# Optimization experiments

Hardware: AMD Instinct MI355X
Metric: run time of the kernel (lower is better)

## Reference

```python
import jax, jax.numpy as jnp
import numpy as np

B, S, D = 2, 2048, 1024
H, HD = 16, 64
FFN_DIM = 4096
EPS = 1e-10


def layer_norm(x, gamma, beta):
    mean = jnp.mean(x, axis=-1, keepdims=True)
    var = jnp.mean((x - mean) ** 2, axis=-1, keepdims=True)
    return (x - mean) / jnp.sqrt(var + EPS) * gamma + beta


def setup_inputs() -> dict:
    key = jax.random.key(0)
    ks = jax.random.split(key, 12)
    s = lambda fan_in, fan_out: (6.0 / (fan_in + fan_out)) ** 0.5
    u = lambda k, shape, c: jax.random.uniform(k, shape, jnp.float32, -c, c)
    return {
        "x": jax.random.normal(ks[0], (B, S, D), jnp.float32),
        "wq": u(ks[1], (H, D, HD), s(D, HD)),
        "bq": jnp.zeros((H, HD), jnp.float32),
        "wk": u(ks[2], (H, D, HD), s(D, HD)),
        "bk": jnp.zeros((H, HD), jnp.float32),
        "wv": u(ks[3], (H, D, HD), s(D, HD)),
        "bv": jnp.zeros((H, HD), jnp.float32),
        "w_proj": u(ks[4], (D, D), s(D, D)),
        "b_proj": jnp.zeros((D,), jnp.float32),
        "gamma1": jnp.ones((D,), jnp.float32),
        "beta1": jnp.zeros((D,), jnp.float32),
        "w1": u(ks[5], (D, FFN_DIM), (1.0 / D) ** 0.5),
        "b1": jnp.zeros((FFN_DIM,), jnp.float32),
        "w2": u(ks[6], (FFN_DIM, D), (1.0 / FFN_DIM) ** 0.5),
        "b2": jnp.zeros((D,), jnp.float32),
        "gamma2": jnp.ones((D,), jnp.float32),
        "beta2": jnp.zeros((D,), jnp.float32),
    }


def reference(x, wq, bq, wk, bk, wv, bv, w_proj, b_proj, gamma1, beta1,
              w1, b1, w2, b2, gamma2, beta2):
    # multi-head self-attention (all heads batched along axis h)
    q = jnp.einsum("bsd,hde->bhse", x, wq) + bq[None, :, None, :]
    k = jnp.einsum("bsd,hde->bhse", x, wk) + bk[None, :, None, :]
    v = jnp.einsum("bsd,hde->bhse", x, wv) + bv[None, :, None, :]
    # scale by sqrt of per-head dim (emb_dim of projected queries)
    scores = jnp.einsum("bhse,bhte->bhst", q, k) / (HD ** 0.5)
    attn = jax.nn.softmax(scores, axis=-1)
    out_h = jnp.einsum("bhst,bhte->bhse", attn, v)  # [B,H,S,HD]
    concat = out_h.transpose(0, 2, 1, 3).reshape(B, S, D)
    attn_out = concat @ w_proj + b_proj
    # residual + norm1 (dropout=0)
    out1 = layer_norm(attn_out + x, gamma1, beta1)
    # FFN: linear - relu - linear
    ffn_out = jax.nn.relu(out1 @ w1 + b1) @ w2 + b2
    # residual + norm2
    return layer_norm(ffn_out + out1, gamma2, beta2)
```

## Files before the change

### kernel.cpp

```cpp
#include <hip/hip_runtime.h>
#include <stdint.h>

typedef float f32x4 __attribute__((ext_vector_type(4)));
typedef __bf16 bf16x8 __attribute__((ext_vector_type(8)));
typedef __bf16 bf16x8_a __attribute__((ext_vector_type(8), may_alias));
typedef __bf16 bf16x4_a __attribute__((ext_vector_type(4), may_alias));
typedef unsigned int u32x4_a __attribute__((ext_vector_type(4), may_alias));
typedef unsigned short u16x4_a __attribute__((ext_vector_type(4), may_alias));

#define DEV __device__ __forceinline__
#define MFMA_B16(a, b, c) __builtin_amdgcn_mfma_f32_16x16x32_bf16((a), (b), (c), 0, 0, 0)

#if __has_builtin(__builtin_amdgcn_exp2f)
#define EXP2(x) __builtin_amdgcn_exp2f(x)
#else
#define EXP2(x) exp2f(x)
#endif

DEV unsigned short f2b(float f) {
  unsigned int u = __float_as_uint(f);
  u = u + 0x7FFFu + ((u >> 16) & 1u);
  return (unsigned short)(u >> 16);
}

#define GLOAD_LDS16(gsrc, ldst)                                                  \
  __builtin_amdgcn_global_load_lds(                                              \
      (__attribute__((address_space(1))) void*)(uintptr_t)(const void*)(gsrc),   \
      (__attribute__((address_space(3))) void*)(ldst), 16, 0, 0)

__global__ __launch_bounds__(256) void cvt_kernel(const float* __restrict__ in,
                                                  unsigned short* __restrict__ out, int n4) {
  int i = blockIdx.x * 256 + threadIdx.x;
  if (i < n4) {
    float4 v = ((const float4*)in)[i];
    u16x4_a t = {f2b(v.x), f2b(v.y), f2b(v.z), f2b(v.w)};
    ((u16x4_a*)out)[i] = t;
  }
}

__global__ __launch_bounds__(256) void transpose_cvt(const float* __restrict__ in,
                                                     unsigned short* __restrict__ out,
                                                     int rows, int cols, float scale) {
  __shared__ float tile[32][33];
  const int tx = threadIdx.x & 31, ty = threadIdx.x >> 5;
  const int c0 = blockIdx.x * 32, r0 = blockIdx.y * 32;
  const float* ip = in + (size_t)blockIdx.z * rows * cols;
  unsigned short* op = out + (size_t)blockIdx.z * rows * cols;
#pragma unroll
  for (int j = 0; j < 32; j += 8)
    tile[ty + j][tx] = ip[(size_t)(r0 + ty + j) * cols + (c0 + tx)];
  __syncthreads();
#pragma unroll
  for (int j = 0; j < 32; j += 8)
    op[(size_t)(c0 + ty + j) * rows + (r0 + tx)] = f2b(tile[tx][ty + j] * scale);
}

__global__ void build_bias_qkv(const float* __restrict__ bq, const float* __restrict__ bk,
                               const float* __restrict__ bv, float* __restrict__ out) {
  int c = blockIdx.x * 256 + threadIdx.x;
  int which = c >> 10, idx = c & 1023;
  float v = which == 0 ? bq[idx] : (which == 1 ? bk[idx] : bv[idx]);
  out[c] = which == 0 ? v * 0.18033688f : v;
}

template <int EP>
__global__ __launch_bounds__(512, 2) void gemm256_kernel(
    const unsigned short* __restrict__ A, const unsigned short* __restrict__ Bt,
    int M, int N, int K, int nbx, int KS,
    const float* __restrict__ bias, unsigned short* __restrict__ outb,
    unsigned short* __restrict__ q_out, unsigned short* __restrict__ k_out,
    unsigned short* __restrict__ v_out,
    float* __restrict__ pp0, float* __restrict__ pp1, float* __restrict__ pp2) {
  __shared__ __align__(16) unsigned short sA[2][256 * 64];
  __shared__ __align__(16) unsigned short sB[2][256 * 64];

  const int tid = threadIdx.x;
  const int wid = tid >> 6, lane = tid & 63;
  const int g = lane >> 4, r15 = lane & 15;
  const int wm = wid >> 2, wn = wid & 3;

  const int nwg = gridDim.x, cpx = nwg >> 3, orig = blockIdx.x;
  const int wg = (orig & 7) * cpx + (orig >> 3);
  const int bx = wg % nbx;
  const int t1 = wg / nbx;
  const int kz = t1 % KS, by = t1 / KS;
  const int row0 = by * 256, col0 = bx * 256;

  const int tilesK = K >> 6;
  const int qT = tilesK / KS, rT = tilesK % KS;
  const int tile0 = kz * qT + (kz < rT ? kz : rT);
  const int NT = qT + (kz < rT ? 1 : 0);
  const int kbase = tile0 << 6;

  const unsigned short* gA0 = A + (size_t)row0 * K + kbase;
  const unsigned short* gB0 = Bt + (size_t)col0 * K + kbase;
  const int srow8 = lane >> 3;
  const int schunk = ((lane & 7) ^ srow8) * 8;

  f32x4 acc[8][4] = {};
  bf16x8 af[4][2], bfr[4][2];

  auto stA = [&](int buf, int k0, int i) {
    const int r = wid * 32 + i * 8;
    GLOAD_LDS16(gA0 + (size_t)(r + srow8) * K + k0 + schunk, &sA[buf][r * 64]);
  };
  auto stB = [&](int buf, int k0, int i) {
    const int r = wid * 32 + i * 8;
    GLOAD_LDS16(gB0 + (size_t)(r + srow8) * K + k0 + schunk, &sB[buf][r * 64]);
  };
  auto ldA = [&](const unsigned short* p, int m, int ks) -> bf16x8 {
    const int row = wm * 128 + m * 16 + r15;
    return *(const bf16x8_a*)&p[row * 64 + (((ks * 4 + g) ^ (r15 & 7)) * 8)];
  };
  auto ldB = [&](const unsigned short* p, int n, int ks) -> bf16x8 {
    const int row = wn * 64 + n * 16 + r15;
    return *(const bf16x8_a*)&p[row * 64 + (((ks * 4 + g) ^ (r15 & 7)) * 8)];
  };

#pragma unroll
  for (int i = 0; i < 4; ++i) { stA(0, 0, i); stB(0, 0, i); }
  asm volatile("s_waitcnt vmcnt(0)" ::: "memory");
  __builtin_amdgcn_s_barrier();

  for (int kt = 0; kt < NT; ++kt) {
    const int cb = kt & 1, nb = cb ^ 1;
    const bool pf = (kt + 1) < NT;
    const int k1 = (kt + 1) << 6;
    const unsigned short* pA = sA[cb];
    const unsigned short* pB = sB[cb];

#pragma unroll
    for (int m = 0; m < 4; ++m) { af[m][0] = ldA(pA, m, 0); af[m][1] = ldA(pA, m, 1); }
#pragma unroll
    for (int n = 0; n < 4; ++n) { bfr[n][0] = ldB(pB, n, 0); bfr[n][1] = ldB(pB, n, 1); }
    if (pf) { stA(nb, k1, 0); stA(nb, k1, 1); }
    __builtin_amdgcn_s_barrier();
    asm volatile("s_waitcnt lgkmcnt(0)" ::: "memory");
    __builtin_amdgcn_sched_barrier(0);
    __builtin_amdgcn_s_setprio(1);
#pragma unroll
    for (int m = 0; m < 4; ++m)
#pragma unroll
      for (int n = 0; n < 2; ++n) {
        acc[m][n] = MFMA_B16(af[m][0], bfr[n][0], acc[m][n]);
        acc[m][n] = MFMA_B16(af[m][1], bfr[n][1], acc[m][n]);
      }
    __builtin_amdgcn_s_setprio(0);
    __builtin_amdgcn_s_barrier();

    if (pf) { stA(nb, k1, 2); stA(nb, k1, 3); }
    __builtin_amdgcn_s_barrier();
    __builtin_amdgcn_s_setprio(1);
#pragma unroll
    for (int m = 0; m < 4; ++m)
#pragma unroll
      for (int n = 2; n < 4; ++n) {
        acc[m][n] = MFMA_B16(af[m][0], bfr[n][0], acc[m][n]);
        acc[m][n] = MFMA_B16(af[m][1], bfr[n][1], acc[m][n]);
      }
    __builtin_amdgcn_s_setprio(0);
    __builtin_amdgcn_s_barrier();

#pragma unroll
    for (int m = 0; m < 4; ++m) { af[m][0] = ldA(pA, m + 4, 0); af[m][1] = ldA(pA, m + 4, 1); }
    if (pf) { stB(nb, k1, 0); stB(nb, k1, 1); }
    __builtin_amdgcn_s_barrier();
    asm volatile("s_waitcnt lgkmcnt(0)" ::: "memory");
    __builtin_amdgcn_sched_barrier(0);
    __builtin_amdgcn_s_setprio(1);
#pragma unroll
    for (int m = 0; m < 4; ++m)
#pragma unroll
      for (int n = 0; n < 2; ++n) {
        acc[m + 4][n] = MFMA_B16(af[m][0], bfr[n][0], acc[m + 4][n]);
        acc[m + 4][n] = MFMA_B16(af[m][1], bfr[n][1], acc[m + 4][n]);
      }
    __builtin_amdgcn_s_setprio(0);
    __builtin_amdgcn_s_barrier();

    if (pf) { stB(nb, k1, 2); stB(nb, k1, 3); }
    __builtin_amdgcn_s_barrier();
    __builtin_amdgcn_s_setprio(1);
#pragma unroll
    for (int m = 0; m < 4; ++m)
#pragma unroll
      for (int n = 2; n < 4; ++n) {
        acc[m + 4][n] = MFMA_B16(af[m][0], bfr[n][0], acc[m + 4][n]);
        acc[m + 4][n] = MFMA_B16(af[m][1], bfr[n][1], acc[m + 4][n]);
      }
    __builtin_amdgcn_s_setprio(0);
    asm volatile("s_waitcnt vmcnt(0)" ::: "memory");
    __builtin_amdgcn_s_barrier();
  }

  float* pz = kz == 0 ? pp0 : (kz == 1 ? pp1 : pp2);
#pragma unroll
  for (int m = 0; m < 8; ++m) {
    const int rbase = row0 + wm * 128 + m * 16 + g * 4;
#pragma unroll
    for (int n = 0; n < 4; ++n) {
      const int col = col0 + wn * 64 + n * 16 + r15;
      const float bb = (EP == 3) ? 0.f : bias[col];
      if constexpr (EP == 0) {
        const int which = col >> 10, cc = col & 1023;
        const int hh = cc >> 6, e = cc & 63;
        const int b = rbase >> 11, s0v = rbase & 2047;
        if (which == 2) {
          bf16x4_a pk;
#pragma unroll
          for (int r = 0; r < 4; ++r) pk[r] = (__bf16)(acc[m][n][r] + bb);
          *(bf16x4_a*)(v_out + (((size_t)(b * 16 + hh) * 64) + e) * 2048 + s0v) = pk;
        } else {
          unsigned short* dst = which == 0 ? q_out : k_out;
#pragma unroll
          for (int r = 0; r < 4; ++r)
            dst[(((size_t)(b * 16 + hh) * 2048) + s0v + r) * 64 + e] =
                f2b(acc[m][n][r] + bb);
        }
      } else {
#pragma unroll
        for (int r = 0; r < 4; ++r) {
          const int row = rbase + r;
          float v = acc[m][n][r] + bb;
          if constexpr (EP == 3) {
            pz[(size_t)row * N + col] = v;
          } else {
            outb[(size_t)row * N + col] = f2b(v > 0.f ? v : 0.f);
          }
        }
      }
    }
  }
}

template <int EP>
__global__ __launch_bounds__(256) void gemm_bt_kernel(
    const unsigned short* __restrict__ A, const unsigned short* __restrict__ Bt,
    int M, int N, int K,
    const float* __restrict__ bias, const float* __restrict__ addf,
    float* __restrict__ outf) {
  __shared__ __align__(16) unsigned short sA[2][128 * 32];
  __shared__ __align__(16) unsigned short sB[2][128 * 32];
  const int tid = threadIdx.x;
  const int wid = tid >> 6, lane = tid & 63;
  const int g = lane >> 4, r15 = lane & 15;
  const int wr = wid >> 1, wc = wid & 1;
  const int row0 = blockIdx.y * 128, col0 = blockIdx.x * 128;

  f32x4 acc[4][4] = {};

  const int c0 = wid * 128 + lane;
  const unsigned short* gA0 = A + (size_t)row0 * K;
  const unsigned short* gB0 = Bt + (size_t)col0 * K;

  auto stage = [&](int buf, int k0) {
#pragma unroll
    for (int j = 0; j < 2; ++j) {
      int c = c0 + j * 64;
      GLOAD_LDS16(gA0 + (size_t)(c >> 2) * K + k0 + (c & 3) * 8,
                  &sA[buf][(wid * 128 + j * 64) * 8]);
      GLOAD_LDS16(gB0 + (size_t)(c >> 2) * K + k0 + (c & 3) * 8,
                  &sB[buf][(wid * 128 + j * 64) * 8]);
    }
  };

  stage(0, 0);
  const int NT = K >> 5;
  for (int t = 0; t < NT; ++t) {
    const int cb = t & 1;
    __syncthreads();
    if (t + 1 < NT) stage(cb ^ 1, (t + 1) * 32);
    bf16x8 af[4], bfr[4];
#pragma unroll
    for (int m = 0; m < 4; ++m)
      af[m] = *(const bf16x8_a*)&sA[cb][(wr * 64 + m * 16 + r15) * 32 + g * 8];
#pragma unroll
    for (int n = 0; n < 4; ++n)
      bfr[n] = *(const bf16x8_a*)&sB[cb][(wc * 64 + n * 16 + r15) * 32 + g * 8];
#pragma unroll
    for (int m = 0; m < 4; ++m)
#pragma unroll
      for (int n = 0; n < 4; ++n)
        acc[m][n] = MFMA_B16(af[m], bfr[n], acc[m][n]);
  }

#pragma unroll
  for (int m = 0; m < 4; ++m) {
    const int rbase = row0 + wr * 64 + m * 16 + g * 4;
#pragma unroll
    for (int n = 0; n < 4; ++n) {
      const int col = col0 + wc * 64 + n * 16 + r15;
      const float bb = bias[col];
#pragma unroll
      for (int r = 0; r < 4; ++r) {
        const int row = rbase + r;
        size_t idx = (size_t)row * N + col;
        outf[idx] = acc[m][n][r] + bb + addf[idx];
      }
    }
  }
}

__global__ __launch_bounds__(256) void attn_kernel(const unsigned short* __restrict__ Q,
                                                   const unsigned short* __restrict__ K,
                                                   const unsigned short* __restrict__ Vt,
                                                   unsigned short* __restrict__ out) {
  const int flat = blockIdx.y * gridDim.x + blockIdx.x;
  const int xcd = flat & 7, rest = flat >> 3;
  const int bh = xcd * 4 + (rest >> 5);
  const int q0 = (rest & 31) * 64;

  const int tid = threadIdx.x, wid = tid >> 6, lane = tid & 63;
  const int g = lane >> 4, r15 = lane & 15;
  const int h = r15 & 7;
  const int s0 = ((g ^ h) * 8);
  const int s1 = (((g + 4) ^ h) * 8);
  const int pswz = r15 & 14;

  __shared__ __align__(16) unsigned short sK[2][64 * 64];
  __shared__ __align__(16) unsigned short sV[2][64 * 64];
  __shared__ __align__(16) unsigned short sP[4][16 * 64];

  const size_t base = (size_t)bh * (2048 * 64);
  const unsigned short* Kb = K + base;
  const unsigned short* Vb = Vt + base;

  const int qrow = q0 + wid * 16 + r15;
  bf16x8 qf[2];
  qf[0] = *(const bf16x8_a*)(Q + base + (size_t)qrow * 64 + g * 8);
  qf[1] = *(const bf16x8_a*)(Q + base + (size_t)qrow * 64 + 32 + g * 8);

  const int srow = lane >> 3;
  const int schunk = ((lane & 7) ^ srow) * 8;

  union {
    unsigned short u[8];
    bf16x8 v;
  } ou;
#pragma unroll
  for (int i = 0; i < 8; ++i) ou.u[i] = 0x3F80;
  const bf16x8 onesb = ou.v;

  f32x4 o[4] = {};
  float mrow = -1e30f, lrow = 0.f;

  auto stage = [&](int bufi, int kt0s) {
#pragma unroll
    for (int i = 0; i < 2; ++i) {
      const int inst = wid * 2 + i;
      const int row = 8 * inst + srow;
      GLOAD_LDS16(Kb + (size_t)(kt0s + row) * 64 + schunk, &sK[bufi][inst * 512]);
      GLOAD_LDS16(Vb + (size_t)row * 2048 + kt0s + schunk, &sV[bufi][inst * 512]);
    }
  };

  stage(0, 0);

  for (int t = 0; t < 32; ++t) {
    const int cur = t & 1;
    __syncthreads();
    if (t < 31) stage(cur ^ 1, (t + 1) * 64);

    f32x4 sc[4] = {};
#pragma unroll
    for (int kt = 0; kt < 4; ++kt) {
      const int rb = (kt * 16 + r15) * 64;
      bf16x8 kf0 = *(const bf16x8_a*)&sK[cur][rb + s0];
      bf16x8 kf1 = *(const bf16x8_a*)&sK[cur][rb + s1];
      sc[kt] = MFMA_B16(kf0, qf[0], sc[kt]);
      sc[kt] = MFMA_B16(kf1, qf[1], sc[kt]);
    }

    float t0 = fmaxf(fmaxf(sc[0][0], sc[0][1]), fmaxf(sc[0][2], sc[0][3]));
    float t1 = fmaxf(fmaxf(sc[1][0], sc[1][1]), fmaxf(sc[1][2], sc[1][3]));
    float t2 = fmaxf(fmaxf(sc[2][0], sc[2][1]), fmaxf(sc[2][2], sc[2][3]));
    float t3 = fmaxf(fmaxf(sc[3][0], sc[3][1]), fmaxf(sc[3][2], sc[3][3]));
    float pmax = fmaxf(fmaxf(t0, t1), fmaxf(t2, t3));
    pmax = fmaxf(pmax, __shfl_xor(pmax, 16));
    pmax = fmaxf(pmax, __shfl_xor(pmax, 32));

    const bool allkeep = __all(pmax - mrow <= 11.5441f);
    float fac;
    if (allkeep) {
      fac = 1.0f;
    } else {
      float nm = fmaxf(mrow, pmax);
      fac = EXP2(mrow - nm);
      mrow = nm;
#pragma unroll
      for (int dt = 0; dt < 4; ++dt)
#pragma unroll
        for (int r = 0; r < 4; ++r) o[dt][r] *= fac;
    }

#pragma unroll
    for (int kt = 0; kt < 4; ++kt) {
      bf16x4_a pb;
      pb[0] = (__bf16)EXP2(sc[kt][0] - mrow);
      pb[1] = (__bf16)EXP2(sc[kt][1] - mrow);
      pb[2] = (__bf16)EXP2(sc[kt][2] - mrow);
      pb[3] = (__bf16)EXP2(sc[kt][3] - mrow);
      *(bf16x4_a*)&sP[wid][r15 * 64 + (((4 * kt + g) ^ pswz) << 2)] = pb;
    }

    bf16x8 pf0 = *(const bf16x8_a*)&sP[wid][r15 * 64 + (((2 * g) ^ pswz) << 2)];
    bf16x8 pf1 = *(const bf16x8_a*)&sP[wid][r15 * 64 + (((8 + 2 * g) ^ pswz) << 2)];

    f32x4 lacc = {};
    lacc = MFMA_B16(onesb, pf0, lacc);
    lacc = MFMA_B16(onesb, pf1, lacc);
    lrow = lrow * fac + lacc[0];

#pragma unroll
    for (int dt = 0; dt < 4; ++dt) {
      const int rb = (dt * 16 + r15) * 64;
      bf16x8 vf0 = *(const bf16x8_a*)&sV[cur][rb + s0];
      bf16x8 vf1 = *(const bf16x8_a*)&sV[cur][rb + s1];
      o[dt] = MFMA_B16(vf0, pf0, o[dt]);
      o[dt] = MFMA_B16(vf1, pf1, o[dt]);
    }
  }

  const int b = bh >> 4, hh = bh & 15;
  const int s = q0 + wid * 16 + r15;
  const float inv = 1.f / lrow;
  unsigned short* orow = out + ((size_t)(b * 2048 + s)) * 1024 + hh * 64;
#pragma unroll
  for (int dt = 0; dt < 4; ++dt) {
    bf16x4_a tq;
    tq[0] = (__bf16)(o[dt][0] * inv);
    tq[1] = (__bf16)(o[dt][1] * inv);
    tq[2] = (__bf16)(o[dt][2] * inv);
    tq[3] = (__bf16)(o[dt][3] * inv);
    *(bf16x4_a*)(orow + dt * 16 + g * 4) = tq;
  }
}

__global__ __launch_bounds__(256) void ln_kernel(const float* __restrict__ in,
                                                 const float* __restrict__ gamma,
                                                 const float* __restrict__ beta,
                                                 float* __restrict__ outf,
                                                 unsigned short* __restrict__ outb) {
  const int row = blockIdx.x, tid = threadIdx.x;
  float4 v = ((const float4*)(in + (size_t)row * 1024))[tid];
  float s = v.x + v.y + v.z + v.w;
  float ss = v.x * v.x + v.y * v.y + v.z * v.z + v.w * v.w;
#pragma unroll
  for (int off = 32; off > 0; off >>= 1) {
    s += __shfl_down(s, off);
    ss += __shfl_down(ss, off);
  }
  __shared__ float red[8];
  const int wid = tid >> 6;
  if ((tid & 63) == 0) { red[wid] = s; red[4 + wid] = ss; }
  __syncthreads();
  float S = red[0] + red[1] + red[2] + red[3];
  float SS = red[4] + red[5] + red[6] + red[7];
  const float mean = S * (1.f / 1024.f);
  const float var = SS * (1.f / 1024.f) - mean * mean;
  const float inv = 1.f / sqrtf(var + 1e-10f);
  float4 gg = ((const float4*)gamma)[tid];
  float4 bb = ((const float4*)beta)[tid];
  float4 o;
  o.x = (v.x - mean) * inv * gg.x + bb.x;
  o.y = (v.y - mean) * inv * gg.y + bb.y;
  o.z = (v.z - mean) * inv * gg.z + bb.z;
  o.w = (v.w - mean) * inv * gg.w + bb.w;
  if (outf) ((float4*)(outf + (size_t)row * 1024))[tid] = o;
  if (outb) {
    u16x4_a t = {f2b(o.x), f2b(o.y), f2b(o.z), f2b(o.w)};
    *(u16x4_a*)(outb + (size_t)row * 1024 + tid * 4) = t;
  }
}

__global__ __launch_bounds__(256) void ln3_kernel(
    const float* __restrict__ p0, const float* __restrict__ p1, const float* __restrict__ p2,
    const float* __restrict__ bias, const float* __restrict__ resid,
    const float* __restrict__ gamma, const float* __restrict__ beta,
    float* __restrict__ outf) {
  const int row = blockIdx.x, tid = threadIdx.x;
  const size_t off = (size_t)row * 1024;
  float4 a = ((const float4*)(p0 + off))[tid];
  float4 b = ((const float4*)(p1 + off))[tid];
  float4 c = ((const float4*)(p2 + off))[tid];
  float4 bb4 = ((const float4*)bias)[tid];
  float4 rr = ((const float4*)(resid + off))[tid];
  float4 v;
  v.x = a.x + b.x + c.x + bb4.x + rr.x;
  v.y = a.y + b.y + c.y + bb4.y + rr.y;
  v.z = a.z + b.z + c.z + bb4.z + rr.z;
  v.w = a.w + b.w + c.w + bb4.w + rr.w;

  float s = v.x + v.y + v.z + v.w;
  float ss = v.x * v.x + v.y * v.y + v.z * v.z + v.w * v.w;
#pragma unroll
  for (int off2 = 32; off2 > 0; off2 >>= 1) {
    s += __shfl_down(s, off2);
    ss += __shfl_down(ss, off2);
  }
  __shared__ float red[8];
  const int wid = tid >> 6;
  if ((tid & 63) == 0) { red[wid] = s; red[4 + wid] = ss; }
  __syncthreads();
  float S = red[0] + red[1] + red[2] + red[3];
  float SS = red[4] + red[5] + red[6] + red[7];
  const float mean = S * (1.f / 1024.f);
  const float var = SS * (1.f / 1024.f) - mean * mean;
  const float inv = 1.f / sqrtf(var + 1e-10f);
  float4 gg = ((const float4*)gamma)[tid];
  float4 be = ((const float4*)beta)[tid];
  float4 o;
  o.x = (v.x - mean) * inv * gg.x + be.x;
  o.y = (v.y - mean) * inv * gg.y + be.y;
  o.z = (v.z - mean) * inv * gg.z + be.z;
  o.w = (v.w - mean) * inv * gg.w + be.w;
  ((float4*)(outf + off))[tid] = o;
}

extern "C" void kernel_launch(void* const* d_in, const int* in_sizes, int n_in,
                              void* d_out, int out_size, void* d_ws, size_t ws_size,
                              hipStream_t stream) {
  const float* x      = (const float*)d_in[0];
  const float* wq     = (const float*)d_in[1];
  const float* bq     = (const float*)d_in[2];
  const float* wk     = (const float*)d_in[3];
  const float* bk     = (const float*)d_in[4];
  const float* wv     = (const float*)d_in[5];
  const float* bv     = (const float*)d_in[6];
  const float* w_proj = (const float*)d_in[7];
  const float* b_proj = (const float*)d_in[8];
  const float* gamma1 = (const float*)d_in[9];
  const float* beta1  = (const float*)d_in[10];
  const float* w1     = (const float*)d_in[11];
  const float* b1     = (const float*)d_in[12];
  const float* w2     = (const float*)d_in[13];
  const float* b2     = (const float*)d_in[14];
  const float* gamma2 = (const float*)d_in[15];
  const float* beta2  = (const float*)d_in[16];

  char* p = (char*)d_ws;
  auto alloc = [&](size_t bytes) {
    char* r = p;
    p += (bytes + 255) & ~(size_t)255;
    return r;
  };
  unsigned short* xb      = (unsigned short*)alloc(4096ull * 1024 * 2);
  unsigned short* Wqkv_t  = (unsigned short*)alloc(3072ull * 1024 * 2);
  unsigned short* Wproj_t = (unsigned short*)alloc(1024ull * 1024 * 2);
  unsigned short* W1t     = (unsigned short*)alloc(4096ull * 1024 * 2);
  unsigned short* W2t     = (unsigned short*)alloc(1024ull * 4096 * 2);
  float*          biasq   = (float*)alloc(3072 * 4);
  unsigned short* Qb      = (unsigned short*)alloc(4096ull * 1024 * 2);
  unsigned short* Kb      = (unsigned short*)alloc(4096ull * 1024 * 2);
  unsigned short* Vtb     = (unsigned short*)alloc(4096ull * 1024 * 2);
  float*          resid1  = (float*)alloc(4096ull * 1024 * 4);
  float*          out1f   = (float*)alloc(4096ull * 1024 * 4);
  unsigned short* out1b   = (unsigned short*)alloc(4096ull * 1024 * 2);
  unsigned short* ffn_h   = (unsigned short*)alloc(4096ull * 4096 * 2);
  unsigned short* concat  = xb;

  float* pp0 = (float*)xb;
  float* pp1 = (float*)Qb;
  float* pp2 = (float*)Vtb;

  cvt_kernel<<<4096, 256, 0, stream>>>(x, xb, 4096 * 1024 / 4);
  transpose_cvt<<<dim3(2, 32, 16), 256, 0, stream>>>(wq, Wqkv_t, 1024, 64, 0.18033688f);
  transpose_cvt<<<dim3(2, 32, 16), 256, 0, stream>>>(wk, Wqkv_t + 1024 * 1024, 1024, 64, 1.f);
  transpose_cvt<<<dim3(2, 32, 16), 256, 0, stream>>>(wv, Wqkv_t + 2048 * 1024, 1024, 64, 1.f);
  transpose_cvt<<<dim3(32, 32, 1), 256, 0, stream>>>(w_proj, Wproj_t, 1024, 1024, 1.f);
  transpose_cvt<<<dim3(128, 32, 1), 256, 0, stream>>>(w1, W1t, 1024, 4096, 1.f);
  transpose_cvt<<<dim3(32, 128, 1), 256, 0, stream>>>(w2, W2t, 4096, 1024, 1.f);
  build_bias_qkv<<<12, 256, 0, stream>>>(bq, bk, bv, biasq);

  gemm256_kernel<0><<<192, 512, 0, stream>>>(xb, Wqkv_t, 4096, 3072, 1024, 12, 1, biasq,
                                             nullptr, Qb, Kb, Vtb, nullptr, nullptr, nullptr);
  attn_kernel<<<dim3(32, 32), 256, 0, stream>>>(Qb, Kb, Vtb, concat);
  gemm_bt_kernel<1><<<dim3(8, 32), 256, 0, stream>>>(concat, Wproj_t, 4096, 1024, 1024, b_proj,
                                                     x, resid1);
  ln_kernel<<<4096, 256, 0, stream>>>(resid1, gamma1, beta1, out1f, out1b);
  gemm256_kernel<2><<<256, 512, 0, stream>>>(out1b, W1t, 4096, 4096, 1024, 16, 1, b1,
                                             ffn_h, nullptr, nullptr, nullptr,
                                             nullptr, nullptr, nullptr);
  gemm256_kernel<3><<<192, 512, 0, stream>>>(ffn_h, W2t, 4096, 1024, 4096, 4, 3, nullptr,
                                             nullptr, nullptr, nullptr, nullptr,
                                             pp0, pp1, pp2);
  ln3_kernel<<<4096, 256, 0, stream>>>(pp0, pp1, pp2, b2, out1f, gamma2, beta2,
                                       (float*)d_out);
}
```

Before: 269.1 us.

## Split-K the output projection and FFN2 GEMMs, fold bias and residual into layernorm

```diff
diff --git a/kernel.cpp b/kernel.cpp
--- a/kernel.cpp
+++ b/kernel.cpp
@@ -70,7 +70,8 @@
     const float* __restrict__ bias, unsigned short* __restrict__ outb,
     unsigned short* __restrict__ q_out, unsigned short* __restrict__ k_out,
     unsigned short* __restrict__ v_out,
-    float* __restrict__ pp0, float* __restrict__ pp1, float* __restrict__ pp2) {
+    float* __restrict__ pp0, float* __restrict__ pp1, float* __restrict__ pp2,
+    float* __restrict__ pp3) {
   __shared__ __align__(16) unsigned short sA[2][256 * 64];
   __shared__ __align__(16) unsigned short sB[2][256 * 64];
 
@@ -193,7 +194,7 @@
     __builtin_amdgcn_s_barrier();
   }
 
-  float* pz = kz == 0 ? pp0 : (kz == 1 ? pp1 : pp2);
+  float* pz = kz == 0 ? pp0 : (kz == 1 ? pp1 : (kz == 2 ? pp2 : pp3));
 #pragma unroll
   for (int m = 0; m < 8; ++m) {
     const int rbase = row0 + wm * 128 + m * 16 + g * 4;
@@ -233,12 +234,10 @@
   }
 }
 
-template <int EP>
 __global__ __launch_bounds__(256) void gemm_bt_kernel(
     const unsigned short* __restrict__ A, const unsigned short* __restrict__ Bt,
-    int M, int N, int K,
-    const float* __restrict__ bias, const float* __restrict__ addf,
-    float* __restrict__ outf) {
+    int M, int N, int Kchunk, int Kstride,
+    float* __restrict__ pp0, float* __restrict__ pp1) {
   __shared__ __align__(16) unsigned short sA[2][128 * 32];
   __shared__ __align__(16) unsigned short sB[2][128 * 32];
   const int tid = threadIdx.x;
@@ -246,26 +245,27 @@
   const int g = lane >> 4, r15 = lane & 15;
   const int wr = wid >> 1, wc = wid & 1;
   const int row0 = blockIdx.y * 128, col0 = blockIdx.x * 128;
+  const int kz = blockIdx.z;
 
   f32x4 acc[4][4] = {};
 
   const int c0 = wid * 128 + lane;
-  const unsigned short* gA0 = A + (size_t)row0 * K;
-  const unsigned short* gB0 = Bt + (size_t)col0 * K;
+  const unsigned short* gA0 = A + (size_t)row0 * Kstride + (size_t)kz * Kchunk;
+  const unsigned short* gB0 = Bt + (size_t)col0 * Kstride + (size_t)kz * Kchunk;
 
   auto stage = [&](int buf, int k0) {
 #pragma unroll
     for (int j = 0; j < 2; ++j) {
       int c = c0 + j * 64;
-      GLOAD_LDS16(gA0 + (size_t)(c >> 2) * K + k0 + (c & 3) * 8,
+      GLOAD_LDS16(gA0 + (size_t)(c >> 2) * Kstride + k0 + (c & 3) * 8,
                   &sA[buf][(wid * 128 + j * 64) * 8]);
-      GLOAD_LDS16(gB0 + (size_t)(c >> 2) * K + k0 + (c & 3) * 8,
+      GLOAD_LDS16(gB0 + (size_t)(c >> 2) * Kstride + k0 + (c & 3) * 8,
                   &sB[buf][(wid * 128 + j * 64) * 8]);
     }
   };
 
   stage(0, 0);
-  const int NT = K >> 5;
+  const int NT = Kchunk >> 5;
   for (int t = 0; t < NT; ++t) {
     const int cb = t & 1;
     __syncthreads();
@@ -284,19 +284,16 @@
         acc[m][n] = MFMA_B16(af[m], bfr[n], acc[m][n]);
   }
 
+  float* pz = kz == 0 ? pp0 : pp1;
 #pragma unroll
   for (int m = 0; m < 4; ++m) {
     const int rbase = row0 + wr * 64 + m * 16 + g * 4;
 #pragma unroll
     for (int n = 0; n < 4; ++n) {
       const int col = col0 + wc * 64 + n * 16 + r15;
-      const float bb = bias[col];
-#pragma unroll
-      for (int r = 0; r < 4; ++r) {
-        const int row = rbase + r;
-        size_t idx = (size_t)row * N + col;
-        outf[idx] = acc[m][n][r] + bb + addf[idx];
-      }
+#pragma unroll
+      for (int r = 0; r < 4; ++r)
+        pz[(size_t)(rbase + r) * N + col] = acc[m][n][r];
     }
   }
 }
@@ -371,11 +368,14 @@
       sc[kt] = MFMA_B16(kf1, qf[1], sc[kt]);
     }
 
-    float t0 = fmaxf(fmaxf(sc[0][0], sc[0][1]), fmaxf(sc[0][2], sc[0][3]));
-    float t1 = fmaxf(fmaxf(sc[1][0], sc[1][1]), fmaxf(sc[1][2], sc[1][3]));
-    float t2 = fmaxf(fmaxf(sc[2][0], sc[2][1]), fmaxf(sc[2][2], sc[2][3]));
-    float t3 = fmaxf(fmaxf(sc[3][0], sc[3][1]), fmaxf(sc[3][2], sc[3][3]));
-    float pmax = fmaxf(fmaxf(t0, t1), fmaxf(t2, t3));
+    float a0 = fmaxf(fmaxf(sc[0][0], sc[0][1]), sc[0][2]);
+    float a1 = fmaxf(fmaxf(sc[0][3], sc[1][0]), sc[1][1]);
+    float a2 = fmaxf(fmaxf(sc[1][2], sc[1][3]), sc[2][0]);
+    float a3 = fmaxf(fmaxf(sc[2][1], sc[2][2]), sc[2][3]);
+    float a4 = fmaxf(fmaxf(sc[3][0], sc[3][1]), sc[3][2]);
+    float b0 = fmaxf(fmaxf(a0, a1), a2);
+    float b1 = fmaxf(fmaxf(a3, a4), sc[3][3]);
+    float pmax = fmaxf(b0, b1);
     pmax = fmaxf(pmax, __shfl_xor(pmax, 16));
     pmax = fmaxf(pmax, __shfl_xor(pmax, 32));
 
@@ -436,19 +436,29 @@
   }
 }
 
-__global__ __launch_bounds__(256) void ln_kernel(const float* __restrict__ in,
-                                                 const float* __restrict__ gamma,
-                                                 const float* __restrict__ beta,
-                                                 float* __restrict__ outf,
-                                                 unsigned short* __restrict__ outb) {
+__global__ __launch_bounds__(256) void ln2p_kernel(
+    const float* __restrict__ p0, const float* __restrict__ p1,
+    const float* __restrict__ bias, const float* __restrict__ resid,
+    const float* __restrict__ gamma, const float* __restrict__ beta,
+    float* __restrict__ outf, unsigned short* __restrict__ outb) {
   const int row = blockIdx.x, tid = threadIdx.x;
-  float4 v = ((const float4*)(in + (size_t)row * 1024))[tid];
+  const size_t off = (size_t)row * 1024;
+  float4 a = ((const float4*)(p0 + off))[tid];
+  float4 b = ((const float4*)(p1 + off))[tid];
+  float4 bb4 = ((const float4*)bias)[tid];
+  float4 rr = ((const float4*)(resid + off))[tid];
+  float4 v;
+  v.x = a.x + b.x + bb4.x + rr.x;
+  v.y = a.y + b.y + bb4.y + rr.y;
+  v.z = a.z + b.z + bb4.z + rr.z;
+  v.w = a.w + b.w + bb4.w + rr.w;
+
   float s = v.x + v.y + v.z + v.w;
   float ss = v.x * v.x + v.y * v.y + v.z * v.z + v.w * v.w;
 #pragma unroll
-  for (int off = 32; off > 0; off >>= 1) {
-    s += __shfl_down(s, off);
-    ss += __shfl_down(ss, off);
+  for (int o2 = 32; o2 > 0; o2 >>= 1) {
+    s += __shfl_down(s, o2);
+    ss += __shfl_down(ss, o2);
   }
   __shared__ float red[8];
   const int wid = tid >> 6;
@@ -460,21 +470,20 @@
   const float var = SS * (1.f / 1024.f) - mean * mean;
   const float inv = 1.f / sqrtf(var + 1e-10f);
   float4 gg = ((const float4*)gamma)[tid];
-  float4 bb = ((const float4*)beta)[tid];
+  float4 be = ((const float4*)beta)[tid];
   float4 o;
-  o.x = (v.x - mean) * inv * gg.x + bb.x;
-  o.y = (v.y - mean) * inv * gg.y + bb.y;
-  o.z = (v.z - mean) * inv * gg.z + bb.z;
-  o.w = (v.w - mean) * inv * gg.w + bb.w;
-  if (outf) ((float4*)(outf + (size_t)row * 1024))[tid] = o;
-  if (outb) {
-    u16x4_a t = {f2b(o.x), f2b(o.y), f2b(o.z), f2b(o.w)};
-    *(u16x4_a*)(outb + (size_t)row * 1024 + tid * 4) = t;
-  }
-}
-
-__global__ __launch_bounds__(256) void ln3_kernel(
-    const float* __restrict__ p0, const float* __restrict__ p1, const float* __restrict__ p2,
+  o.x = (v.x - mean) * inv * gg.x + be.x;
+  o.y = (v.y - mean) * inv * gg.y + be.y;
+  o.z = (v.z - mean) * inv * gg.z + be.z;
+  o.w = (v.w - mean) * inv * gg.w + be.w;
+  ((float4*)(outf + off))[tid] = o;
+  u16x4_a t = {f2b(o.x), f2b(o.y), f2b(o.z), f2b(o.w)};
+  *(u16x4_a*)(outb + off + tid * 4) = t;
+}
+
+__global__ __launch_bounds__(256) void ln4p_kernel(
+    const float* __restrict__ p0, const float* __restrict__ p1,
+    const float* __restrict__ p2, const float* __restrict__ p3,
     const float* __restrict__ bias, const float* __restrict__ resid,
     const float* __restrict__ gamma, const float* __restrict__ beta,
     float* __restrict__ outf) {
@@ -483,20 +492,21 @@
   float4 a = ((const float4*)(p0 + off))[tid];
   float4 b = ((const float4*)(p1 + off))[tid];
   float4 c = ((const float4*)(p2 + off))[tid];
+  float4 d = ((const float4*)(p3 + off))[tid];
   float4 bb4 = ((const float4*)bias)[tid];
   float4 rr = ((const float4*)(resid + off))[tid];
   float4 v;
-  v.x = a.x + b.x + c.x + bb4.x + rr.x;
-  v.y = a.y + b.y + c.y + bb4.y + rr.y;
-  v.z = a.z + b.z + c.z + bb4.z + rr.z;
-  v.w = a.w + b.w + c.w + bb4.w + rr.w;
+  v.x = (a.x + b.x) + (c.x + d.x) + bb4.x + rr.x;
+  v.y = (a.y + b.y) + (c.y + d.y) + bb4.y + rr.y;
+  v.z = (a.z + b.z) + (c.z + d.z) + bb4.z + rr.z;
+  v.w = (a.w + b.w) + (c.w + d.w) + bb4.w + rr.w;
 
   float s = v.x + v.y + v.z + v.w;
   float ss = v.x * v.x + v.y * v.y + v.z * v.z + v.w * v.w;
 #pragma unroll
-  for (int off2 = 32; off2 > 0; off2 >>= 1) {
-    s += __shfl_down(s, off2);
-    ss += __shfl_down(ss, off2);
+  for (int o2 = 32; o2 > 0; o2 >>= 1) {
+    s += __shfl_down(s, o2);
+    ss += __shfl_down(ss, o2);
   }
   __shared__ float red[8];
   const int wid = tid >> 6;
@@ -547,21 +557,24 @@
   unsigned short* xb      = (unsigned short*)alloc(4096ull * 1024 * 2);
   unsigned short* Wqkv_t  = (unsigned short*)alloc(3072ull * 1024 * 2);
   unsigned short* Wproj_t = (unsigned short*)alloc(1024ull * 1024 * 2);
-  unsigned short* W1t     = (unsigned short*)alloc(4096ull * 1024 * 2);
   unsigned short* W2t     = (unsigned short*)alloc(1024ull * 4096 * 2);
   float*          biasq   = (float*)alloc(3072 * 4);
   unsigned short* Qb      = (unsigned short*)alloc(4096ull * 1024 * 2);
   unsigned short* Kb      = (unsigned short*)alloc(4096ull * 1024 * 2);
   unsigned short* Vtb     = (unsigned short*)alloc(4096ull * 1024 * 2);
+  unsigned short* W1t     = (unsigned short*)alloc(4096ull * 1024 * 2);
   float*          resid1  = (float*)alloc(4096ull * 1024 * 4);
   float*          out1f   = (float*)alloc(4096ull * 1024 * 4);
   unsigned short* out1b   = (unsigned short*)alloc(4096ull * 1024 * 2);
   unsigned short* ffn_h   = (unsigned short*)alloc(4096ull * 4096 * 2);
   unsigned short* concat  = xb;
 
+  float* prA = (float*)Qb;
+  float* prB = resid1;
   float* pp0 = (float*)xb;
   float* pp1 = (float*)Qb;
   float* pp2 = (float*)Vtb;
+  float* pp3 = resid1;
 
   cvt_kernel<<<4096, 256, 0, stream>>>(x, xb, 4096 * 1024 / 4);
   transpose_cvt<<<dim3(2, 32, 16), 256, 0, stream>>>(wq, Wqkv_t, 1024, 64, 0.18033688f);
@@ -573,17 +586,18 @@
   build_bias_qkv<<<12, 256, 0, stream>>>(bq, bk, bv, biasq);
 
   gemm256_kernel<0><<<192, 512, 0, stream>>>(xb, Wqkv_t, 4096, 3072, 1024, 12, 1, biasq,
-                                             nullptr, Qb, Kb, Vtb, nullptr, nullptr, nullptr);
+                                             nullptr, Qb, Kb, Vtb, nullptr, nullptr,
+                                             nullptr, nullptr);
   attn_kernel<<<dim3(32, 32), 256, 0, stream>>>(Qb, Kb, Vtb, concat);
-  gemm_bt_kernel<1><<<dim3(8, 32), 256, 0, stream>>>(concat, Wproj_t, 4096, 1024, 1024, b_proj,
-                                                     x, resid1);
-  ln_kernel<<<4096, 256, 0, stream>>>(resid1, gamma1, beta1, out1f, out1b);
+  gemm_bt_kernel<<<dim3(8, 32, 2), 256, 0, stream>>>(concat, Wproj_t, 4096, 1024, 512, 1024,
+                                                     prA, prB);
+  ln2p_kernel<<<4096, 256, 0, stream>>>(prA, prB, b_proj, x, gamma1, beta1, out1f, out1b);
   gemm256_kernel<2><<<256, 512, 0, stream>>>(out1b, W1t, 4096, 4096, 1024, 16, 1, b1,
                                              ffn_h, nullptr, nullptr, nullptr,
-                                             nullptr, nullptr, nullptr);
-  gemm256_kernel<3><<<192, 512, 0, stream>>>(ffn_h, W2t, 4096, 1024, 4096, 4, 3, nullptr,
+                                             nullptr, nullptr, nullptr, nullptr);
+  gemm256_kernel<3><<<256, 512, 0, stream>>>(ffn_h, W2t, 4096, 1024, 4096, 4, 4, nullptr,
                                              nullptr, nullptr, nullptr, nullptr,
-                                             pp0, pp1, pp2);
-  ln3_kernel<<<4096, 256, 0, stream>>>(pp0, pp1, pp2, b2, out1f, gamma2, beta2,
-                                       (float*)d_out);
-}
+                                             pp0, pp1, pp2, pp3);
+  ln4p_kernel<<<4096, 256, 0, stream>>>(pp0, pp1, pp2, pp3, b2, out1f, gamma2, beta2,
+                                        (float*)d_out);
+}
```

Result: faster. 263.6 us (-2.1%).
